# Performance work log

Hardware: AMD Instinct MI355X
Metric: run time of the kernel (lower is better)

## Reference

```python
import jax, jax.numpy as jnp
import numpy as np

NUM_NODES = 100_000
NUM_EDGES = 3_200_000
NUM_GRAPHS = 200
F_IN = 128
HID = 64
BN_EPS = 1e-5


def setup_inputs() -> dict:
    key = jax.random.key(0)
    ks = jax.random.split(key, 12)
    x = jax.random.normal(ks[0], (NUM_NODES, F_IN), dtype=jnp.float32)
    edge_index = jax.random.randint(ks[1], (2, NUM_EDGES), 0, NUM_NODES, dtype=jnp.int64)
    batch = jnp.sort(jax.random.randint(ks[2], (NUM_NODES,), 0, NUM_GRAPHS, dtype=jnp.int64))
    s1 = float(np.sqrt(6.0 / F_IN))  # kaiming_uniform-ish bound
    s2 = float(np.sqrt(6.0 / HID))
    W1 = jax.random.uniform(ks[3], (HID, F_IN), jnp.float32, -s1, s1)
    b1 = jnp.zeros((HID,), jnp.float32)
    W2 = jax.random.uniform(ks[4], (HID, HID), jnp.float32, -s2, s2)
    b2 = jnp.zeros((HID,), jnp.float32)
    gamma1 = jnp.ones((HID,), jnp.float32)
    beta1 = jnp.zeros((HID,), jnp.float32)
    mean1 = 0.1 * jax.random.normal(ks[5], (HID,), jnp.float32)
    var1 = jax.random.uniform(ks[6], (HID,), jnp.float32, 0.5, 1.5)
    gamma2 = jnp.ones((HID,), jnp.float32)
    beta2 = jnp.zeros((HID,), jnp.float32)
    mean2 = 0.1 * jax.random.normal(ks[7], (HID,), jnp.float32)
    var2 = jax.random.uniform(ks[8], (HID,), jnp.float32, 0.5, 1.5)
    Wl = jax.random.uniform(ks[9], (1, HID), jnp.float32, -s2, s2)
    bl = jnp.zeros((1,), jnp.float32)
    return dict(x=x, edge_index=edge_index, batch=batch,
                W1=W1, b1=b1, gamma1=gamma1, beta1=beta1, mean1=mean1, var1=var1,
                W2=W2, b2=b2, gamma2=gamma2, beta2=beta2, mean2=mean2, var2=var2,
                Wl=Wl, bl=bl)


def _gcn_conv(x, W, b, src, dst, dinv):
    # PyG GCNConv: h = x @ W.T, then D^{-1/2}(A+I)D^{-1/2} aggregation, then + bias
    h = x @ W.T                                    # [N, out]
    w_edge = (dinv[src] * dinv[dst])[:, None]      # [E, 1]
    msg = h[src] * w_edge                          # [E, out] gather
    agg = jax.ops.segment_sum(msg, dst, num_segments=NUM_NODES)
    agg = agg + h * (dinv * dinv)[:, None]         # self-loop term
    return agg + b


def _bn_eval(h, gamma, beta, mean, var):
    return (h - mean) * (gamma * jax.lax.rsqrt(var + BN_EPS)) + beta


def reference(x, edge_index, batch,
              W1, b1, gamma1, beta1, mean1, var1,
              W2, b2, gamma2, beta2, mean2, var2,
              Wl, bl):
    src, dst = edge_index[0], edge_index[1]
    # degrees over A + I (self-loops add 1)
    deg = jax.ops.segment_sum(jnp.ones((NUM_EDGES,), jnp.float32), dst,
                              num_segments=NUM_NODES) + 1.0
    dinv = jax.lax.rsqrt(deg)
    h = jax.nn.relu(_bn_eval(_gcn_conv(x, W1, b1, src, dst, dinv),
                             gamma1, beta1, mean1, var1))
    # dropout = identity (eval mode)
    h = jax.nn.relu(_bn_eval(_gcn_conv(h, W2, b2, src, dst, dinv),
                             gamma2, beta2, mean2, var2))
    # global_mean_pool over graph ids
    sums = jax.ops.segment_sum(h, batch, num_segments=NUM_GRAPHS)
    cnts = jax.ops.segment_sum(jnp.ones((NUM_NODES,), jnp.float32), batch,
                               num_segments=NUM_GRAPHS)
    pooled = sums / jnp.maximum(cnts, 1.0)[:, None]  # [G, 64]
    return pooled @ Wl.T + bl                        # [G, 1]
```

## Files before the change

kernel.cpp:

```cpp
#include <hip/hip_runtime.h>
#include <hip/hip_bf16.h>

#define NN 100000
#define FF 128
#define HH 64
#define BN_EPS 1e-5f

__global__ void k_detect(const unsigned* __restrict__ ei, int* __restrict__ flag) {
    if (threadIdx.x == 0 && blockIdx.x == 0) {
        unsigned o = 0;
        for (int i = 1; i < 32; i += 2) o |= ei[i];
        *flag = (o == 0) ? 1 : 0;
    }
}

__device__ __forceinline__ int load_idx(const void* p, int i, int is64) {
    return is64 ? (int)((const long long*)p)[i] : ((const int*)p)[i];
}

__global__ void k_count(const void* __restrict__ ei, int E, const int* __restrict__ flag,
                        int* __restrict__ counts) {
    int e = blockIdx.x * blockDim.x + threadIdx.x;
    if (e >= E) return;
    int is64 = *flag;
    int d = load_idx(ei, E + e, is64);
    atomicAdd(&counts[d], 1);
}

__global__ void k_dinv(const int* __restrict__ counts, float* __restrict__ dinv,
                       const void* __restrict__ bat, const int* __restrict__ flag,
                       int* __restrict__ gcnt, int N) {
    int i = blockIdx.x * blockDim.x + threadIdx.x;
    if (i >= N) return;
    float deg = (float)counts[i] + 1.0f;
    dinv[i] = rsqrtf(deg);
    int is64 = *flag;
    int b = load_idx(bat, i, is64);
    atomicAdd(&gcnt[b], 1);
}

__global__ void k_scan1(const int* __restrict__ counts, int* __restrict__ partial, int N) {
    __shared__ int s[512];
    int t = threadIdx.x;
    int i = blockIdx.x * 512 + t;
    int v = (i < N) ? counts[i] : 0;
    s[t] = v; __syncthreads();
    for (int off = 256; off; off >>= 1) {
        if (t < off) s[t] += s[t + off];
        __syncthreads();
    }
    if (t == 0) partial[blockIdx.x] = s[0];
}

__global__ void k_scan2(int* __restrict__ partial, int nch) {
    __shared__ int s[256];
    int t = threadIdx.x;
    int v = (t < nch) ? partial[t] : 0;
    s[t] = v; __syncthreads();
    for (int off = 1; off < 256; off <<= 1) {
        int add = (t >= off) ? s[t - off] : 0;
        __syncthreads();
        s[t] += add;
        __syncthreads();
    }
    if (t < nch) partial[t] = s[t] - v;
}

__global__ void k_scan3(const int* __restrict__ counts, const int* __restrict__ partial,
                        int* __restrict__ rp, int N, int E) {
    __shared__ int s[512];
    int t = threadIdx.x;
    int i = blockIdx.x * 512 + t;
    int v = (i < N) ? counts[i] : 0;
    s[t] = v; __syncthreads();
    for (int off = 1; off < 512; off <<= 1) {
        int add = (t >= off) ? s[t - off] : 0;
        __syncthreads();
        s[t] += add;
        __syncthreads();
    }
    if (i < N) rp[i] = partial[blockIdx.x] + s[t] - v;
    if (i == N) rp[N] = E;
}

__global__ void k_fill(const void* __restrict__ ei, int E, const int* __restrict__ flag,
                       const float* __restrict__ dinv, const int* __restrict__ rp,
                       int* __restrict__ fillcnt, int2* __restrict__ cw) {
    int e = blockIdx.x * blockDim.x + threadIdx.x;
    if (e >= E) return;
    int is64 = *flag;
    int s = load_idx(ei, e, is64);
    int d = load_idx(ei, E + e, is64);
    float w = dinv[s] * dinv[d];
    int pos = rp[d] + atomicAdd(&fillcnt[d], 1);
    int2 p; p.x = s; p.y = __float_as_int(w);
    cw[pos] = p;
}

__global__ void k_prep(const float* b1, const float* g1, const float* be1,
                       const float* m1, const float* v1,
                       const float* b2, const float* g2, const float* be2,
                       const float* m2, const float* v2,
                       float* sc1, float* sh1, float* sc2, float* sh2) {
    int f = threadIdx.x;
    if (f < HH) {
        float s1 = g1[f] * rsqrtf(v1[f] + BN_EPS);
        sc1[f] = s1; sh1[f] = (b1[f] - m1[f]) * s1 + be1[f];
        float s2 = g2[f] * rsqrtf(v2[f] + BN_EPS);
        sc2[f] = s2; sh2[f] = (b2[f] - m2[f]) * s2 + be2[f];
    }
}

template <int K, int NPB>
__global__ void k_gemm(const float* __restrict__ x, const float* __restrict__ W,
                       float* __restrict__ out, int N) {
    __shared__ float wT[K * (HH + 1)];
    __shared__ float xs[NPB * K];
    const int TB = NPB * 64;
    int t = threadIdx.x;
    for (int idx = t; idx < K * HH; idx += TB) {
        int f = idx / K, k = idx % K;
        wT[k * (HH + 1) + f] = W[idx];
    }
    int nb = blockIdx.x * NPB;
    for (int idx = t; idx < NPB * K; idx += TB) {
        int gi = nb * K + idx;
        xs[idx] = (gi < N * K) ? x[gi] : 0.0f;
    }
    __syncthreads();
    int f = t & 63, nl = t >> 6;
    float acc = 0.0f;
#pragma unroll
    for (int k = 0; k < K; k++)
        acc += xs[nl * K + k] * wT[k * (HH + 1) + f];
    int n = nb + nl;
    if (n < N) out[n * HH + f] = acc;
}

template <int LAYER>
__global__ void k_agg(const float* __restrict__ h, const int2* __restrict__ cw,
                      const int* __restrict__ rp, const float* __restrict__ dinv,
                      const float* __restrict__ sc, const float* __restrict__ sh,
                      float* __restrict__ out,
                      const void* __restrict__ bat, const int* __restrict__ flag,
                      const float* __restrict__ Wl, float* __restrict__ gsum, int N) {
    int wid = (int)((blockIdx.x * blockDim.x + threadIdx.x) >> 6);
    if (wid >= N) return;
    int lane = threadIdx.x & 63;
    int q = lane >> 4;
    int fl = lane & 15;
    const float4* __restrict__ h4 = (const float4*)h;

    int s = rp[wid], e = rp[wid + 1];
    float ax = 0.f, ay = 0.f, az = 0.f, aw = 0.f;

    for (int base = s; base < e; base += 64) {
        int navail = e - base; if (navail > 64) navail = 64;
        int li = base + (lane < navail ? lane : navail - 1);
        int2 pk = cw[li];
        int   slane = pk.x;
        float wlane = (lane < navail) ? __int_as_float(pk.y) : 0.f;
        for (int g = 0; g < navail; g += 8) {
            int i0 = g + q, i1 = g + 4 + q;
            int s0 = __shfl(slane, i0);
            int s1 = __shfl(slane, i1);
            float w0 = __shfl(wlane, i0);
            float w1 = __shfl(wlane, i1);
            float4 r0 = h4[s0 * 16 + fl];
            float4 r1 = h4[s1 * 16 + fl];
            ax += w0 * r0.x + w1 * r1.x;
            ay += w0 * r0.y + w1 * r1.y;
            az += w0 * r0.z + w1 * r1.z;
            aw += w0 * r0.w + w1 * r1.w;
        }
    }
    ax += __shfl_xor(ax, 16); ay += __shfl_xor(ay, 16);
    az += __shfl_xor(az, 16); aw += __shfl_xor(aw, 16);
    ax += __shfl_xor(ax, 32); ay += __shfl_xor(ay, 32);
    az += __shfl_xor(az, 32); aw += __shfl_xor(aw, 32);

    float di = dinv[wid];
    float di2 = di * di;
    float4 sr = h4[wid * 16 + fl];
    ax += di2 * sr.x; ay += di2 * sr.y; az += di2 * sr.z; aw += di2 * sr.w;

    int f0 = fl * 4;
    float vx = fmaxf(ax * sc[f0 + 0] + sh[f0 + 0], 0.f);
    float vy = fmaxf(ay * sc[f0 + 1] + sh[f0 + 1], 0.f);
    float vz = fmaxf(az * sc[f0 + 2] + sh[f0 + 2], 0.f);
    float vw = fmaxf(aw * sc[f0 + 3] + sh[f0 + 3], 0.f);

    if (LAYER == 1) {
        if (lane < 16) {
            float4 o; o.x = vx; o.y = vy; o.z = vz; o.w = vw;
            ((float4*)out)[wid * 16 + fl] = o;
        }
    } else {
        float tval = vx * Wl[f0] + vy * Wl[f0 + 1] + vz * Wl[f0 + 2] + vw * Wl[f0 + 3];
        tval += __shfl_xor(tval, 1);
        tval += __shfl_xor(tval, 2);
        tval += __shfl_xor(tval, 4);
        tval += __shfl_xor(tval, 8);
        if (lane == 0) {
            int is64 = *flag;
            int b = load_idx(bat, wid, is64);
            atomicAdd(&gsum[b], tval);
        }
    }
}

__global__ void k_final(const float* __restrict__ gsum, const int* __restrict__ gcnt,
                        const float* __restrict__ bl, float* __restrict__ outp, int G) {
    int g = blockIdx.x * blockDim.x + threadIdx.x;
    if (g < G) outp[g] = gsum[g] / fmaxf((float)gcnt[g], 1.0f) + bl[0];
}

extern "C" void kernel_launch(void* const* d_in, const int* in_sizes, int n_in,
                              void* d_out, int out_size, void* d_ws, size_t ws_size,
                              hipStream_t stream) {
    const float* x   = (const float*)d_in[0];
    const void*  ei  = d_in[1];
    const void*  bat = d_in[2];
    const float* W1  = (const float*)d_in[3];
    const float* b1  = (const float*)d_in[4];
    const float* g1  = (const float*)d_in[5];
    const float* be1 = (const float*)d_in[6];
    const float* m1  = (const float*)d_in[7];
    const float* v1  = (const float*)d_in[8];
    const float* W2  = (const float*)d_in[9];
    const float* b2  = (const float*)d_in[10];
    const float* g2  = (const float*)d_in[11];
    const float* be2 = (const float*)d_in[12];
    const float* m2  = (const float*)d_in[13];
    const float* v2  = (const float*)d_in[14];
    const float* Wl  = (const float*)d_in[15];
    const float* bl  = (const float*)d_in[16];
    float* outp = (float*)d_out;

    const int N = NN;
    const int E = in_sizes[1] / 2;
    const int G = out_size;

    char* base = (char*)d_ws;
    size_t off = 0;
    auto alloc = [&](size_t bytes) { void* p = base + off; off = (off + bytes + 255) & ~(size_t)255; return p; };
    int*   flag    = (int*)  alloc(16);
    float* dinv    = (float*)alloc((size_t)N * 4);
    int*   counts  = (int*)  alloc((size_t)N * 4);
    int*   rp      = (int*)  alloc(((size_t)N + 1) * 4);
    int*   fillcnt = (int*)  alloc((size_t)N * 4);
    int*   partial = (int*)  alloc(1024);
    float* sc1     = (float*)alloc(HH * 4);
    float* sh1     = (float*)alloc(HH * 4);
    float* sc2     = (float*)alloc(HH * 4);
    float* sh2     = (float*)alloc(HH * 4);
    float* gsum    = (float*)alloc((size_t)G * 4);
    int*   gcnt    = (int*)  alloc((size_t)G * 4);
    int2*  cw      = (int2*) alloc((size_t)E * 8);
    float* bufA    = (float*)alloc((size_t)N * HH * 4);
    float* bufB    = (float*)alloc((size_t)N * HH * 4);
    (void)ws_size;

    hipMemsetAsync(counts, 0, (size_t)N * 4, stream);
    hipMemsetAsync(fillcnt, 0, (size_t)N * 4, stream);
    hipMemsetAsync(gsum, 0, (size_t)G * 4, stream);
    hipMemsetAsync(gcnt, 0, (size_t)G * 4, stream);

    k_detect<<<1, 64, 0, stream>>>((const unsigned*)ei, flag);

    int eb = (E + 255) / 256;
    k_count<<<eb, 256, 0, stream>>>(ei, E, flag, counts);

    int nb = (N + 255) / 256;
    k_dinv<<<nb, 256, 0, stream>>>(counts, dinv, bat, flag, gcnt, N);

    int nch = (N + 511) / 512;
    k_scan1<<<nch, 512, 0, stream>>>(counts, partial, N);
    k_scan2<<<1, 256, 0, stream>>>(partial, nch);
    k_scan3<<<nch, 512, 0, stream>>>(counts, partial, rp, N, E);

    k_fill<<<eb, 256, 0, stream>>>(ei, E, flag, dinv, rp, fillcnt, cw);

    k_prep<<<1, 64, 0, stream>>>(b1, g1, be1, m1, v1, b2, g2, be2, m2, v2,
                                 sc1, sh1, sc2, sh2);

    k_gemm<FF, 8><<<(N + 7) / 8, 512, 0, stream>>>(x, W1, bufA, N);
    k_agg<1><<<(N + 3) / 4, 256, 0, stream>>>(bufA, cw, rp, dinv, sc1, sh1, bufB,
                                              bat, flag, Wl, gsum, N);
    k_gemm<HH, 8><<<(N + 7) / 8, 512, 0, stream>>>(bufB, W2, bufA, N);
    k_agg<2><<<(N + 3) / 4, 256, 0, stream>>>(bufA, cw, rp, dinv, sc2, sh2, nullptr,
                                              bat, flag, Wl, gsum, N);

    k_final<<<1, 256, 0, stream>>>(gsum, gcnt, bl, outp, G);
}
```

Measured before the change: 1.224 ms.

## Store layer-1 features as bf16 feature slabs and aggregate in four cache-friendly passes

The first GEMM now writes its output as bf16, split into four 16-feature slabs. The layer-1 aggregation runs one pass per slab, so each pass gathers from a much smaller table that can stay in cache, and each gathered row is half the size. The cost is re-reading the CSR edge list four times, plus the accuracy loss from rounding intermediate features to bf16. Layer 2 keeps the fp32 path.

New measurement: 1.310 ms. +7.1%, slower.

```diff
diff --git a/kernel.cpp b/kernel.cpp
--- a/kernel.cpp
+++ b/kernel.cpp
@@ -5,6 +5,14 @@
 #define FF 128
 #define HH 64
 #define BN_EPS 1e-5f
+
+typedef unsigned int uint_t;
+
+__device__ __forceinline__ float bflo(uint_t u) { return __uint_as_float(u << 16); }
+__device__ __forceinline__ float bfhi(uint_t u) { return __uint_as_float(u & 0xFFFF0000u); }
+__device__ __forceinline__ unsigned short f2bf(float f) {
+    uint_t a = __float_as_uint(f); a += 0x7FFF + ((a >> 16) & 1); return (unsigned short)(a >> 16);
+}
 
 __global__ void k_detect(const unsigned* __restrict__ ei, int* __restrict__ flag) {
     if (threadIdx.x == 0 && blockIdx.x == 0) {
@@ -112,6 +120,32 @@
 }
 
 template <int K, int NPB>
+__global__ void k_gemmQ(const float* __restrict__ x, const float* __restrict__ W,
+                        unsigned short* __restrict__ outq, int N) {
+    __shared__ float wT[K * (HH + 1)];
+    __shared__ float xs[NPB * K];
+    const int TB = NPB * 64;
+    int t = threadIdx.x;
+    for (int idx = t; idx < K * HH; idx += TB) {
+        int f = idx / K, k = idx % K;
+        wT[k * (HH + 1) + f] = W[idx];
+    }
+    int nb = blockIdx.x * NPB;
+    for (int idx = t; idx < NPB * K; idx += TB) {
+        int gi = nb * K + idx;
+        xs[idx] = (gi < N * K) ? x[gi] : 0.0f;
+    }
+    __syncthreads();
+    int f = t & 63, nl = t >> 6;
+    float acc = 0.0f;
+#pragma unroll
+    for (int k = 0; k < K; k++)
+        acc += xs[nl * K + k] * wT[k * (HH + 1) + f];
+    int n = nb + nl;
+    if (n < N) outq[(size_t)(f >> 4) * (N * 16) + n * 16 + (f & 15)] = f2bf(acc);
+}
+
+template <int K, int NPB>
 __global__ void k_gemm(const float* __restrict__ x, const float* __restrict__ W,
                        float* __restrict__ out, int N) {
     __shared__ float wT[K * (HH + 1)];
@@ -137,11 +171,65 @@
     if (n < N) out[n * HH + f] = acc;
 }
 
-template <int LAYER>
+__global__ void k_aggQ(const unsigned short* __restrict__ hq, const int2* __restrict__ cw,
+                       const int* __restrict__ rp, const float* __restrict__ dinv,
+                       const float* __restrict__ sc, const float* __restrict__ sh,
+                       float* __restrict__ out, int N) {
+    int pass = blockIdx.y;
+    int wid = (int)((blockIdx.x * blockDim.x + threadIdx.x) >> 6);
+    if (wid >= N) return;
+    int lane = threadIdx.x & 63;
+    int slot = lane >> 2;
+    int c    = lane & 3;
+    const uint2* __restrict__ hp = (const uint2*)hq + (size_t)pass * N * 4;
+
+    int s = rp[wid], e = rp[wid + 1];
+    float a0 = 0.f, a1 = 0.f, a2 = 0.f, a3 = 0.f;
+
+    for (int base = s; base < e; base += 64) {
+        int navail = e - base; if (navail > 64) navail = 64;
+        int li = base + (lane < navail ? lane : navail - 1);
+        long long pkv = __builtin_nontemporal_load((const long long*)cw + li);
+        int   slane = (int)(pkv & 0xFFFFFFFFll);
+        int   wbits = (int)(pkv >> 32);
+        float wlane = (lane < navail) ? __int_as_float(wbits) : 0.f;
+        for (int g = 0; g < navail; g += 32) {
+            int i0 = g + slot, i1 = g + 16 + slot;
+            int s0 = __shfl(slane, i0);
+            int s1 = __shfl(slane, i1);
+            float w0 = __shfl(wlane, i0);
+            float w1 = __shfl(wlane, i1);
+            uint2 r0 = hp[(size_t)s0 * 4 + c];
+            uint2 r1 = hp[(size_t)s1 * 4 + c];
+            a0 += w0 * bflo(r0.x) + w1 * bflo(r1.x);
+            a1 += w0 * bfhi(r0.x) + w1 * bfhi(r1.x);
+            a2 += w0 * bflo(r0.y) + w1 * bflo(r1.y);
+            a3 += w0 * bfhi(r0.y) + w1 * bfhi(r1.y);
+        }
+    }
+#pragma unroll
+    for (int off = 4; off <= 32; off <<= 1) {
+        a0 += __shfl_xor(a0, off); a1 += __shfl_xor(a1, off);
+        a2 += __shfl_xor(a2, off); a3 += __shfl_xor(a3, off);
+    }
+    if (lane < 4) {
+        float di = dinv[wid], di2 = di * di;
+        uint2 sr = hp[(size_t)wid * 4 + c];
+        a0 += di2 * bflo(sr.x); a1 += di2 * bfhi(sr.x);
+        a2 += di2 * bflo(sr.y); a3 += di2 * bfhi(sr.y);
+        int f0 = pass * 16 + c * 4;
+        float4 o;
+        o.x = fmaxf(a0 * sc[f0 + 0] + sh[f0 + 0], 0.f);
+        o.y = fmaxf(a1 * sc[f0 + 1] + sh[f0 + 1], 0.f);
+        o.z = fmaxf(a2 * sc[f0 + 2] + sh[f0 + 2], 0.f);
+        o.w = fmaxf(a3 * sc[f0 + 3] + sh[f0 + 3], 0.f);
+        ((float4*)out)[(size_t)wid * 16 + pass * 4 + c] = o;
+    }
+}
+
 __global__ void k_agg(const float* __restrict__ h, const int2* __restrict__ cw,
                       const int* __restrict__ rp, const float* __restrict__ dinv,
                       const float* __restrict__ sc, const float* __restrict__ sh,
-                      float* __restrict__ out,
                       const void* __restrict__ bat, const int* __restrict__ flag,
                       const float* __restrict__ Wl, float* __restrict__ gsum, int N) {
     int wid = (int)((blockIdx.x * blockDim.x + threadIdx.x) >> 6);
@@ -190,22 +278,15 @@
     float vz = fmaxf(az * sc[f0 + 2] + sh[f0 + 2], 0.f);
     float vw = fmaxf(aw * sc[f0 + 3] + sh[f0 + 3], 0.f);
 
-    if (LAYER == 1) {
-        if (lane < 16) {
-            float4 o; o.x = vx; o.y = vy; o.z = vz; o.w = vw;
-            ((float4*)out)[wid * 16 + fl] = o;
-        }
-    } else {
-        float tval = vx * Wl[f0] + vy * Wl[f0 + 1] + vz * Wl[f0 + 2] + vw * Wl[f0 + 3];
-        tval += __shfl_xor(tval, 1);
-        tval += __shfl_xor(tval, 2);
-        tval += __shfl_xor(tval, 4);
-        tval += __shfl_xor(tval, 8);
-        if (lane == 0) {
-            int is64 = *flag;
-            int b = load_idx(bat, wid, is64);
-            atomicAdd(&gsum[b], tval);
-        }
+    float tval = vx * Wl[f0] + vy * Wl[f0 + 1] + vz * Wl[f0 + 2] + vw * Wl[f0 + 3];
+    tval += __shfl_xor(tval, 1);
+    tval += __shfl_xor(tval, 2);
+    tval += __shfl_xor(tval, 4);
+    tval += __shfl_xor(tval, 8);
+    if (lane == 0) {
+        int is64 = *flag;
+        int b = load_idx(bat, wid, is64);
+        atomicAdd(&gsum[b], tval);
     }
 }
 
@@ -257,6 +338,7 @@
     float* gsum    = (float*)alloc((size_t)G * 4);
     int*   gcnt    = (int*)  alloc((size_t)G * 4);
     int2*  cw      = (int2*) alloc((size_t)E * 8);
+    unsigned short* hq = (unsigned short*)alloc((size_t)N * HH * 2);
     float* bufA    = (float*)alloc((size_t)N * HH * 4);
     float* bufB    = (float*)alloc((size_t)N * HH * 4);
     (void)ws_size;
@@ -284,12 +366,13 @@
     k_prep<<<1, 64, 0, stream>>>(b1, g1, be1, m1, v1, b2, g2, be2, m2, v2,
                                  sc1, sh1, sc2, sh2);
 
-    k_gemm<FF, 8><<<(N + 7) / 8, 512, 0, stream>>>(x, W1, bufA, N);
-    k_agg<1><<<(N + 3) / 4, 256, 0, stream>>>(bufA, cw, rp, dinv, sc1, sh1, bufB,
-                                              bat, flag, Wl, gsum, N);
-    k_gemm<HH, 8><<<(N + 7) / 8, 512, 0, stream>>>(bufB, W2, bufA, N);
-    k_agg<2><<<(N + 3) / 4, 256, 0, stream>>>(bufA, cw, rp, dinv, sc2, sh2, nullptr,
-                                              bat, flag, Wl, gsum, N);
+    k_gemmQ<FF, 8><<<(N + 7) / 8, 512, 0, stream>>>(x, W1, hq, N);
+    dim3 agrid1((N + 3) / 4, 4);
+    k_aggQ<<<agrid1, 256, 0, stream>>>(hq, cw, rp, dinv, sc1, sh1, bufA, N);
+
+    k_gemm<HH, 8><<<(N + 7) / 8, 512, 0, stream>>>(bufA, W2, bufB, N);
+    k_agg<<<(N + 3) / 4, 256, 0, stream>>>(bufB, cw, rp, dinv, sc2, sh2,
+                                           bat, flag, Wl, gsum, N);
 
     k_final<<<1, 256, 0, stream>>>(gsum, gcnt, bl, outp, G);
 }
```
